# Optimization experiments

Hardware: AMD Instinct MI355X
Metric: run time of the kernel (lower is better)

Reference implementation:

```python
import jax, jax.numpy as jnp
import numpy as np

NUM_LAYER = 4
EMB = 64
ATOM_VOCAB = 64
BOND_VOCAB = 8
BN_EPS = 1e-5


def _batchnorm(h, gamma, beta):
    m = h.mean(axis=0)
    v = h.var(axis=0)
    return gamma * (h - m) * jax.lax.rsqrt(v + BN_EPS) + beta


def setup_inputs() -> dict:
    key = jax.random.key(0)
    ks = jax.random.split(key, 16)
    N, E, L = 100000, 1000000, NUM_LAYER
    x = jax.random.randint(ks[0], (N, 9), 0, ATOM_VOCAB)
    edge_index = jax.random.randint(ks[1], (2, E), 0, N)
    edge_attr = jax.random.randint(ks[2], (E, 3), 0, BOND_VOCAB)
    batch = jnp.sort(jax.random.randint(ks[3], (N,), 0, 512))
    s = 0.02
    atom_emb = jax.random.normal(ks[4], (9, ATOM_VOCAB, EMB), jnp.float32) * s
    bond_emb = jax.random.normal(ks[5], (L, 3, BOND_VOCAB, EMB), jnp.float32) * s
    eps = jnp.zeros((L,), jnp.float32)
    W1 = jax.random.normal(ks[6], (L, EMB, 2 * EMB), jnp.float32) * s
    b1 = jnp.zeros((L, 2 * EMB), jnp.float32)
    bn1_g = jnp.ones((L, 2 * EMB), jnp.float32)
    bn1_b = jnp.zeros((L, 2 * EMB), jnp.float32)
    W2 = jax.random.normal(ks[7], (L, 2 * EMB, EMB), jnp.float32) * s
    b2 = jnp.zeros((L, EMB), jnp.float32)
    bn_g = jnp.ones((L, EMB), jnp.float32)
    bn_b = jnp.zeros((L, EMB), jnp.float32)
    return dict(x=x, edge_index=edge_index, edge_attr=edge_attr, batch=batch,
                atom_emb=atom_emb, bond_emb=bond_emb, eps=eps,
                W1=W1, b1=b1, bn1_g=bn1_g, bn1_b=bn1_b,
                W2=W2, b2=b2, bn_g=bn_g, bn_b=bn_b)


def reference(x, edge_index, edge_attr, batch, atom_emb, bond_emb, eps,
              W1, b1, bn1_g, bn1_b, W2, b2, bn_g, bn_b):
    N = x.shape[0]
    src, dst = edge_index[0], edge_index[1]
    # AtomEncoder: sum embeddings over the 9 atom-feature columns
    h = sum(atom_emb[c][x[:, c]] for c in range(9))  # [N, EMB]
    for layer in range(NUM_LAYER):
        # BondEncoder for this layer
        ee = sum(bond_emb[layer, c][edge_attr[:, c]] for c in range(3))  # [E, EMB]
        # message: relu(x_j + edge_emb); aggregate: scatter-add at dst
        msg = jax.nn.relu(h[src] + ee)
        agg = jax.ops.segment_sum(msg, dst, num_segments=N)
        z = (1.0 + eps[layer]) * h + agg
        # MLP: Linear -> BN -> ReLU -> Linear
        z = z @ W1[layer] + b1[layer]
        z = jax.nn.relu(_batchnorm(z, bn1_g[layer], bn1_b[layer]))
        z = z @ W2[layer] + b2[layer]
        # outer BatchNorm, then ReLU on all but last layer (dropout = identity)
        z = _batchnorm(z, bn_g[layer], bn_b[layer])
        if layer < NUM_LAYER - 1:
            z = jax.nn.relu(z)
        h = z
    return (h, batch)
```

## Files before the change

kernel.cpp:

```cpp
#include <hip/hip_runtime.h>
#include <hip/hip_bf16.h>

#define N_NODES 100000
#define N_EDGES 1000000
#define EMB 64
#define NLAYER 4
#define NTILE 1563
#define NSB 391
#define NSHARD 16

typedef __hip_bfloat16 bf16;
typedef __attribute__((ext_vector_type(8))) short short8;
typedef __attribute__((ext_vector_type(4))) float f32x4;

static __device__ __forceinline__ float b2f(bf16 v) { return __bfloat162float(v); }
static __device__ __forceinline__ bf16 f2b(float v) { return __float2bfloat16(v); }

__global__ void k_atom(const int* __restrict__ x, const bf16* __restrict__ aemb,
                       bf16* __restrict__ P) {
    int tid = blockIdx.x * 256 + threadIdx.x;
    int n = tid >> 6, e = tid & 63;
    float s = 0.f;
#pragma unroll
    for (int c = 0; c < 9; ++c) {
        int v = x[n * 9 + c];
        s += b2f(aemb[(c * 64 + v) * 64 + e]);
    }
    P[tid] = f2b(s);
}

__global__ void k_bond(const bf16* __restrict__ bemb, bf16* __restrict__ cb) {
    int idx = blockIdx.x * 256 + threadIdx.x;
    int l = idx >> 15, r = idx & 32767;
    int combo = r >> 6, c = r & 63;
    int e0 = combo & 7, e1 = (combo >> 3) & 7, e2 = combo >> 6;
    float v = b2f(bemb[((l * 3 + 0) * 8 + e0) * 64 + c]) +
              b2f(bemb[((l * 3 + 1) * 8 + e1) * 64 + c]) +
              b2f(bemb[((l * 3 + 2) * 8 + e2) * 64 + c]);
    cb[idx] = f2b(v);
}

__global__ void k_hist(const int* __restrict__ ei, int* __restrict__ deg) {
    int e = blockIdx.x * 256 + threadIdx.x;
    if (e < N_EDGES) atomicAdd(&deg[ei[N_EDGES + e]], 1);
}

__global__ void k_scanA(const int* __restrict__ deg, int* __restrict__ bsum) {
    __shared__ int red[256];
    int i = blockIdx.x * 256 + threadIdx.x;
    red[threadIdx.x] = (i < N_NODES) ? deg[i] : 0;
    __syncthreads();
    for (int d = 128; d > 0; d >>= 1) {
        if (threadIdx.x < d) red[threadIdx.x] += red[threadIdx.x + d];
        __syncthreads();
    }
    if (threadIdx.x == 0) bsum[blockIdx.x] = red[0];
}

__global__ void k_scanB(const int* __restrict__ bsum, int* __restrict__ boff,
                        int* __restrict__ offs) {
    __shared__ int s[512];
    int t = threadIdx.x;
    s[t] = (t < NSB) ? bsum[t] : 0;
    __syncthreads();
    for (int d = 1; d < 512; d <<= 1) {
        int v = (t >= d) ? s[t - d] : 0;
        __syncthreads();
        s[t] += v;
        __syncthreads();
    }
    if (t < NSB) boff[t] = s[t] - bsum[t];
    if (t == 0) offs[N_NODES] = s[NSB - 1];
}

__global__ void k_scanC(const int* __restrict__ deg, const int* __restrict__ boff,
                        int* __restrict__ offs, int* __restrict__ cursor) {
    __shared__ int s[256];
    int i = blockIdx.x * 256 + threadIdx.x;
    int t = threadIdx.x;
    int d0 = (i < N_NODES) ? deg[i] : 0;
    s[t] = d0;
    __syncthreads();
    for (int d = 1; d < 256; d <<= 1) {
        int v = (t >= d) ? s[t - d] : 0;
        __syncthreads();
        s[t] += v;
        __syncthreads();
    }
    if (i < N_NODES) {
        int off = boff[blockIdx.x] + s[t] - d0;
        offs[i] = off;
        cursor[i] = off;
    }
}

__global__ void k_bucket(const int* __restrict__ ei, const int* __restrict__ ea,
                         int* __restrict__ cursor, int2* __restrict__ csr) {
    int e = blockIdx.x * 256 + threadIdx.x;
    if (e < N_EDGES) {
        int d = ei[N_EDGES + e];
        int pos = atomicAdd(&cursor[d], 1);
        int pk = ea[e * 3] + (ea[e * 3 + 1] << 3) + (ea[e * 3 + 2] << 6);
        csr[pos] = make_int2(ei[e], pk);
    }
}

__global__ void k_agg(const bf16* __restrict__ P, const int* __restrict__ offs,
                      const int2* __restrict__ csr,
                      const bf16* __restrict__ cb, const bf16* __restrict__ eps,
                      const float* __restrict__ p2s, const bf16* __restrict__ g2,
                      const bf16* __restrict__ bb2, int layer,
                      bf16* __restrict__ G, float* __restrict__ p1s) {
    if (blockIdx.x < NSHARD) p1s[blockIdx.x * 256 + threadIdx.x] = 0.f;
    int tid = blockIdx.x * 256 + threadIdx.x;
    int c = tid & 63;
    int n = __builtin_amdgcn_readfirstlane(tid >> 6);
    float av = 1.f, cv = 0.f, lo = -3.4e38f;
    if (layer > 0) {
        const float* pp = p2s + (layer - 1) * NSHARD * 128;
        float S = 0.f, Q = 0.f;
#pragma unroll
        for (int s = 0; s < NSHARD; ++s) { S += pp[s * 128 + c]; Q += pp[s * 128 + 64 + c]; }
        float mean = S / (float)N_NODES;
        float var = fmaxf(Q / (float)N_NODES - mean * mean, 0.f);
        av = b2f(g2[(layer - 1) * 64 + c]) * rsqrtf(var + 1e-5f);
        cv = b2f(bb2[(layer - 1) * 64 + c]) - mean * av;
        lo = 0.f;
    }
    const bf16* cbl = cb + layer * 512 * 64;
    float hself = fmaxf(av * b2f(P[(size_t)n * 64 + c]) + cv, lo);
    float acc = (1.f + b2f(eps[layer])) * hself;
    int s0 = __builtin_amdgcn_readfirstlane(offs[n]);
    int s1 = __builtin_amdgcn_readfirstlane(offs[n + 1]);
    int i = s0;
    for (; i + 8 <= s1; i += 8) {
        int sr[8], ep[8];
        float hv[8], bv[8];
#pragma unroll
        for (int u = 0; u < 8; ++u) {
            int2 ed = csr[i + u];
            sr[u] = __builtin_amdgcn_readfirstlane(ed.x);
            ep[u] = __builtin_amdgcn_readfirstlane(ed.y);
        }
#pragma unroll
        for (int u = 0; u < 8; ++u) hv[u] = b2f(P[(size_t)sr[u] * 64 + c]);
#pragma unroll
        for (int u = 0; u < 8; ++u) bv[u] = b2f(cbl[(size_t)ep[u] * 64 + c]);
#pragma unroll
        for (int u = 0; u < 8; ++u)
            acc += fmaxf(fmaxf(av * hv[u] + cv, lo) + bv[u], 0.f);
    }
    for (; i + 4 <= s1; i += 4) {
        int sr[4], ep[4];
        float hv[4], bv[4];
#pragma unroll
        for (int u = 0; u < 4; ++u) {
            int2 ed = csr[i + u];
            sr[u] = __builtin_amdgcn_readfirstlane(ed.x);
            ep[u] = __builtin_amdgcn_readfirstlane(ed.y);
        }
#pragma unroll
        for (int u = 0; u < 4; ++u) hv[u] = b2f(P[(size_t)sr[u] * 64 + c]);
#pragma unroll
        for (int u = 0; u < 4; ++u) bv[u] = b2f(cbl[(size_t)ep[u] * 64 + c]);
#pragma unroll
        for (int u = 0; u < 4; ++u)
            acc += fmaxf(fmaxf(av * hv[u] + cv, lo) + bv[u], 0.f);
    }
    for (; i < s1; ++i) {
        int2 ed = csr[i];
        int sr = __builtin_amdgcn_readfirstlane(ed.x);
        int ep = __builtin_amdgcn_readfirstlane(ed.y);
        float m = fmaxf(av * b2f(P[(size_t)sr * 64 + c]) + cv, lo) +
                  b2f(cbl[(size_t)ep * 64 + c]);
        acc += fmaxf(m, 0.f);
    }
    G[tid] = f2b(acc);
}

__global__ void k_wt(const bf16* __restrict__ W1, const bf16* __restrict__ W2,
                     bf16* __restrict__ W1T, bf16* __restrict__ W2T) {
    int idx = blockIdx.x * 256 + threadIdx.x;
    int l = idx >> 13, r = idx & 8191;
    int k = r >> 7, n = r & 127;
    W1T[l * 8192 + n * 64 + k] = W1[idx];
    int k2 = r >> 6, n2 = r & 63;
    W2T[l * 8192 + n2 * 128 + k2] = W2[idx];
}

__global__ __launch_bounds__(256) void k_mlp1s(
    const bf16* __restrict__ X, const bf16* __restrict__ W1T, const bf16* __restrict__ b1,
    int layer, float* __restrict__ p1s, float* __restrict__ p2s) {
    __shared__ bf16 zt[64 * 72];
    __shared__ float ps[4][4][32];
    __shared__ float qs[4][4][32];
    if (blockIdx.x < NSHARD && threadIdx.x < 128)
        p2s[(layer * NSHARD + blockIdx.x) * 128 + threadIdx.x] = 0.f;
    const bf16* Wl = W1T + layer * 8192;
    int r0 = blockIdx.x * 64;
    int nrows = min(64, N_NODES - r0);
    for (int i = threadIdx.x; i < 512; i += 256) {
        int r = i >> 3, c = (i & 7) * 8;
        short8 v = {};
        if (r < nrows) v = *(const short8*)&X[(r0 + r) * 64 + c];
        *(short8*)&zt[r * 72 + c] = v;
    }
    __syncthreads();
    int wid = threadIdx.x >> 6;
    int l = threadIdx.x & 63;
    int l15 = l & 15, lq = l >> 4;
    f32x4 acc[4][2];
#pragma unroll
    for (int m = 0; m < 4; ++m)
#pragma unroll
        for (int n = 0; n < 2; ++n) acc[m][n] = (f32x4){0.f, 0.f, 0.f, 0.f};
#pragma unroll
    for (int s = 0; s < 2; ++s) {
        short8 a[4], b[2];
#pragma unroll
        for (int m = 0; m < 4; ++m)
            a[m] = *(const short8*)&zt[(m * 16 + l15) * 72 + s * 32 + lq * 8];
#pragma unroll
        for (int n = 0; n < 2; ++n)
            b[n] = *(const short8*)&Wl[(wid * 32 + n * 16 + l15) * 64 + s * 32 + lq * 8];
#pragma unroll
        for (int m = 0; m < 4; ++m)
#pragma unroll
            for (int n = 0; n < 2; ++n)
                acc[m][n] = __builtin_amdgcn_mfma_f32_16x16x32_bf16(a[m], b[n], acc[m][n], 0, 0, 0);
    }
    float bb[2], cs[2] = {0.f, 0.f}, cq[2] = {0.f, 0.f};
#pragma unroll
    for (int n = 0; n < 2; ++n) bb[n] = b2f(b1[layer * 128 + wid * 32 + n * 16 + l15]);
#pragma unroll
    for (int m = 0; m < 4; ++m)
#pragma unroll
        for (int r = 0; r < 4; ++r) {
            int row = m * 16 + lq * 4 + r;
            if (row < nrows) {
#pragma unroll
                for (int n = 0; n < 2; ++n) {
                    float v = acc[m][n][r] + bb[n];
                    cs[n] += v; cq[n] += v * v;
                }
            }
        }
#pragma unroll
    for (int n = 0; n < 2; ++n) {
        ps[wid][lq][n * 16 + l15] = cs[n];
        qs[wid][lq][n * 16 + l15] = cq[n];
    }
    __syncthreads();
    if (threadIdx.x < 128) {
        int t = threadIdx.x, ww = t >> 5, cc = t & 31;
        float S = 0.f, Q = 0.f;
#pragma unroll
        for (int s4 = 0; s4 < 4; ++s4) { S += ps[ww][s4][cc]; Q += qs[ww][s4][cc]; }
        int sh = blockIdx.x & (NSHARD - 1);
        atomicAdd(&p1s[sh * 256 + t], S);
        atomicAdd(&p1s[sh * 256 + 128 + t], Q);
    }
}

__global__ __launch_bounds__(256) void k_mlp2(
    const bf16* __restrict__ W1T, const bf16* __restrict__ b1,
    const bf16* __restrict__ g1, const bf16* __restrict__ bb1,
    const float* __restrict__ p1s,
    const bf16* __restrict__ W2T, const bf16* __restrict__ bias2, int layer,
    const bf16* __restrict__ X, bf16* __restrict__ Y, float* __restrict__ p2s) {
    __shared__ bf16 zt[64 * 72];
    __shared__ bf16 yt[64 * 136];
    __shared__ float ps2[4][4][16];
    __shared__ float qs2[4][4][16];
    const bf16* W1l = W1T + layer * 8192;
    const bf16* W2l = W2T + layer * 8192;
    int r0 = blockIdx.x * 64;
    int nrows = min(64, N_NODES - r0);
    for (int i = threadIdx.x; i < 512; i += 256) {
        int r = i >> 3, c = (i & 7) * 8;
        short8 v = {};
        if (r < nrows) v = *(const short8*)&X[(r0 + r) * 64 + c];
        *(short8*)&zt[r * 72 + c] = v;
    }
    __syncthreads();
    int wid = threadIdx.x >> 6;
    int l = threadIdx.x & 63;
    int l15 = l & 15, lq = l >> 4;
    {
        f32x4 acc[4][2];
#pragma unroll
        for (int m = 0; m < 4; ++m)
#pragma unroll
            for (int n = 0; n < 2; ++n) acc[m][n] = (f32x4){0.f, 0.f, 0.f, 0.f};
#pragma unroll
        for (int s = 0; s < 2; ++s) {
            short8 a[4], b[2];
#pragma unroll
            for (int m = 0; m < 4; ++m)
                a[m] = *(const short8*)&zt[(m * 16 + l15) * 72 + s * 32 + lq * 8];
#pragma unroll
            for (int n = 0; n < 2; ++n)
                b[n] = *(const short8*)&W1l[(wid * 32 + n * 16 + l15) * 64 + s * 32 + lq * 8];
#pragma unroll
            for (int m = 0; m < 4; ++m)
#pragma unroll
                for (int n = 0; n < 2; ++n)
                    acc[m][n] = __builtin_amdgcn_mfma_f32_16x16x32_bf16(a[m], b[n], acc[m][n], 0, 0, 0);
        }
        float aav[2], ccv[2], bbv[2];
#pragma unroll
        for (int n = 0; n < 2; ++n) {
            int col = wid * 32 + n * 16 + l15;
            float S = 0.f, Q = 0.f;
#pragma unroll
            for (int s4 = 0; s4 < NSHARD; ++s4) {
                S += p1s[s4 * 256 + col];
                Q += p1s[s4 * 256 + 128 + col];
            }
            float mean = S / (float)N_NODES;
            float var = fmaxf(Q / (float)N_NODES - mean * mean, 0.f);
            aav[n] = b2f(g1[layer * 128 + col]) * rsqrtf(var + 1e-5f);
            ccv[n] = b2f(bb1[layer * 128 + col]) - mean * aav[n];
            bbv[n] = b2f(b1[layer * 128 + col]);
        }
#pragma unroll
        for (int m = 0; m < 4; ++m)
#pragma unroll
            for (int n = 0; n < 2; ++n)
#pragma unroll
                for (int r = 0; r < 4; ++r) {
                    int row = m * 16 + lq * 4 + r;
                    float v = fmaxf(aav[n] * (acc[m][n][r] + bbv[n]) + ccv[n], 0.f);
                    yt[row * 136 + wid * 32 + n * 16 + l15] = f2b(v);
                }
    }
    __syncthreads();
    {
        f32x4 acc2[4];
#pragma unroll
        for (int m = 0; m < 4; ++m) acc2[m] = (f32x4){0.f, 0.f, 0.f, 0.f};
#pragma unroll
        for (int s = 0; s < 4; ++s) {
            short8 a[4];
            short8 b = *(const short8*)&W2l[(wid * 16 + l15) * 128 + s * 32 + lq * 8];
#pragma unroll
            for (int m = 0; m < 4; ++m)
                a[m] = *(const short8*)&yt[(m * 16 + l15) * 136 + s * 32 + lq * 8];
#pragma unroll
            for (int m = 0; m < 4; ++m)
                acc2[m] = __builtin_amdgcn_mfma_f32_16x16x32_bf16(a[m], b, acc2[m], 0, 0, 0);
        }
        float bb2 = b2f(bias2[layer * 64 + wid * 16 + l15]);
        float cs = 0.f, cq = 0.f;
#pragma unroll
        for (int m = 0; m < 4; ++m)
#pragma unroll
            for (int r = 0; r < 4; ++r) {
                int row = m * 16 + lq * 4 + r;
                float v = acc2[m][r] + bb2;
                zt[row * 72 + wid * 16 + l15] = f2b(v);
                if (row < nrows) { cs += v; cq += v * v; }
            }
        ps2[wid][lq][l15] = cs;
        qs2[wid][lq][l15] = cq;
    }
    __syncthreads();
    for (int i = threadIdx.x; i < 512; i += 256) {
        int r = i >> 3, c = (i & 7) * 8;
        if (r < nrows)
            *(short8*)&Y[(r0 + r) * 64 + c] = *(const short8*)&zt[r * 72 + c];
    }
    if (threadIdx.x < 64) {
        int ww = threadIdx.x >> 4, cc = threadIdx.x & 15;
        float S = 0.f, Q = 0.f;
#pragma unroll
        for (int s4 = 0; s4 < 4; ++s4) { S += ps2[ww][s4][cc]; Q += qs2[ww][s4][cc]; }
        int sh = blockIdx.x & (NSHARD - 1);
        atomicAdd(&p2s[(layer * NSHARD + sh) * 128 + threadIdx.x], S);
        atomicAdd(&p2s[(layer * NSHARD + sh) * 128 + 64 + threadIdx.x], Q);
    }
}

__global__ void k_out(const bf16* __restrict__ P, const float* __restrict__ p2s,
                      const bf16* __restrict__ g2, const bf16* __restrict__ bb2,
                      const int* __restrict__ batch, float* __restrict__ out) {
    int tid = blockIdx.x * 256 + threadIdx.x;
    int c = tid & 63;
    const float* pp = p2s + 3 * NSHARD * 128;
    float S = 0.f, Q = 0.f;
#pragma unroll
    for (int s = 0; s < NSHARD; ++s) { S += pp[s * 128 + c]; Q += pp[s * 128 + 64 + c]; }
    float mean = S / (float)N_NODES;
    float var = fmaxf(Q / (float)N_NODES - mean * mean, 0.f);
    float av = b2f(g2[3 * 64 + c]) * rsqrtf(var + 1e-5f);
    float cv = b2f(bb2[3 * 64 + c]) - mean * av;
    float v = b2f(f2b(av * b2f(P[tid]) + cv));
    out[tid] = (v != v || fabsf(v) > 1e20f) ? 0.f : v;
    if (tid < N_NODES) out[N_NODES * EMB + tid] = (float)batch[tid];
}

extern "C" void kernel_launch(void* const* d_in, const int* in_sizes, int n_in,
                              void* d_out, int out_size, void* d_ws, size_t ws_size,
                              hipStream_t stream) {
    (void)in_sizes; (void)n_in; (void)out_size; (void)ws_size;
    const int* x     = (const int*)d_in[0];
    const int* ei    = (const int*)d_in[1];
    const int* ea    = (const int*)d_in[2];
    const int* batch = (const int*)d_in[3];
    const bf16* aemb = (const bf16*)d_in[4];
    const bf16* bemb = (const bf16*)d_in[5];
    const bf16* eps  = (const bf16*)d_in[6];
    const bf16* W1   = (const bf16*)d_in[7];
    const bf16* b1   = (const bf16*)d_in[8];
    const bf16* g1   = (const bf16*)d_in[9];
    const bf16* bb1  = (const bf16*)d_in[10];
    const bf16* W2   = (const bf16*)d_in[11];
    const bf16* b2   = (const bf16*)d_in[12];
    const bf16* g2   = (const bf16*)d_in[13];
    const bf16* bb2  = (const bf16*)d_in[14];

    bf16* Y = (bf16*)d_ws;
    char* ob = (char*)d_out;
    bf16* X       = (bf16*)ob;
    int*  deg     = (int*)(ob + 12800000);
    int*  offs    = (int*)(ob + 13200000);
    int*  cursor  = (int*)(ob + 13600008);
    int2* csr     = (int2*)(ob + 14000008);
    float* p1s    = (float*)(ob + 22000008);
    float* p2s    = (float*)(ob + 22016392);
    int*  bsum    = (int*)(ob + 22049160);
    int*  boff    = (int*)(ob + 22050724);
    bf16* w1t     = (bf16*)(ob + 22052288);
    bf16* w2t     = (bf16*)(ob + 22117824);
    bf16* cbt     = (bf16*)(ob + 22183360);

    hipMemsetAsync(deg, 0, 400000, stream);

    k_atom<<<25000, 256, 0, stream>>>(x, aemb, Y);
    k_wt<<<128, 256, 0, stream>>>(W1, W2, w1t, w2t);
    k_bond<<<512, 256, 0, stream>>>(bemb, cbt);
    k_hist<<<3907, 256, 0, stream>>>(ei, deg);
    k_scanA<<<NSB, 256, 0, stream>>>(deg, bsum);
    k_scanB<<<1, 512, 0, stream>>>(bsum, boff, offs);
    k_scanC<<<NSB, 256, 0, stream>>>(deg, boff, offs, cursor);
    k_bucket<<<3907, 256, 0, stream>>>(ei, ea, cursor, csr);

    for (int l = 0; l < NLAYER; ++l) {
        k_agg<<<25000, 256, 0, stream>>>(Y, offs, csr, cbt, eps,
                                         p2s, g2, bb2, l, X, p1s);
        k_mlp1s<<<NTILE, 256, 0, stream>>>(X, w1t, b1, l, p1s, p2s);
        k_mlp2<<<NTILE, 256, 0, stream>>>(w1t, b1, g1, bb1, p1s, w2t, b2, l, X, Y, p2s);
    }
    k_out<<<25000, 256, 0, stream>>>(Y, p2s, g2, bb2, batch, (float*)d_out);
}
```

Before: 574.1 us.

## Build CSR via two-pass binned scatter to localize random writes

Replaces the single-pass random atomic bucket scatter with a two-pass scheme. Edges are first grouped into coarse destination bins of 512 nodes, using per-block shared-memory counts and global bin cursors. A per-bin pass then does the fine scatter into the CSR, so the cursor atomics and CSR writes stay within a small address range per block. This adds an extra pass over the edge data, a temporary buffer, and bin histogram and scan work.

After: 586.1 us. 2.1% more time.

```diff
diff --git a/kernel.cpp b/kernel.cpp
--- a/kernel.cpp
+++ b/kernel.cpp
@@ -8,6 +8,8 @@
 #define NTILE 1563
 #define NSB 391
 #define NSHARD 16
+#define NBIN 196
+#define NS1B 489
 
 typedef __hip_bfloat16 bf16;
 typedef __attribute__((ext_vector_type(8))) short short8;
@@ -40,9 +42,21 @@
     cb[idx] = f2b(v);
 }
 
-__global__ void k_hist(const int* __restrict__ ei, int* __restrict__ deg) {
-    int e = blockIdx.x * 256 + threadIdx.x;
-    if (e < N_EDGES) atomicAdd(&deg[ei[N_EDGES + e]], 1);
+__global__ __launch_bounds__(1024) void k_hist(const int* __restrict__ ei,
+                                               int* __restrict__ deg,
+                                               int* __restrict__ bcnt) {
+    __shared__ int lb[NBIN];
+    for (int i = threadIdx.x; i < NBIN; i += 1024) lb[i] = 0;
+    __syncthreads();
+    int e = blockIdx.x * 1024 + threadIdx.x;
+    if (e < N_EDGES) {
+        int d = ei[N_EDGES + e];
+        atomicAdd(&deg[d], 1);
+        atomicAdd(&lb[d >> 9], 1);
+    }
+    __syncthreads();
+    for (int i = threadIdx.x; i < NBIN; i += 1024)
+        if (lb[i]) atomicAdd(&bcnt[i], lb[i]);
 }
 
 __global__ void k_scanA(const int* __restrict__ deg, int* __restrict__ bsum) {
@@ -58,19 +72,24 @@
 }
 
 __global__ void k_scanB(const int* __restrict__ bsum, int* __restrict__ boff,
-                        int* __restrict__ offs) {
-    __shared__ int s[512];
+                        int* __restrict__ offs, const int* __restrict__ bcnt,
+                        int* __restrict__ bbase, int* __restrict__ bcur) {
+    __shared__ int s[512], s2[512];
     int t = threadIdx.x;
-    s[t] = (t < NSB) ? bsum[t] : 0;
+    int v0 = (t < NSB) ? bsum[t] : 0;
+    int b0 = (t < NBIN) ? bcnt[t] : 0;
+    s[t] = v0; s2[t] = b0;
     __syncthreads();
     for (int d = 1; d < 512; d <<= 1) {
-        int v = (t >= d) ? s[t - d] : 0;
+        int va = (t >= d) ? s[t - d] : 0;
+        int vb = (t >= d) ? s2[t - d] : 0;
         __syncthreads();
-        s[t] += v;
+        s[t] += va; s2[t] += vb;
         __syncthreads();
     }
-    if (t < NSB) boff[t] = s[t] - bsum[t];
+    if (t < NSB) boff[t] = s[t] - v0;
     if (t == 0) offs[N_NODES] = s[NSB - 1];
+    if (t < NBIN) { int st = s2[t] - b0; bbase[t] = st; bcur[t] = st; }
 }
 
 __global__ void k_scanC(const int* __restrict__ deg, const int* __restrict__ boff,
@@ -94,14 +113,53 @@
     }
 }
 
-__global__ void k_bucket(const int* __restrict__ ei, const int* __restrict__ ea,
-                         int* __restrict__ cursor, int2* __restrict__ csr) {
-    int e = blockIdx.x * 256 + threadIdx.x;
-    if (e < N_EDGES) {
-        int d = ei[N_EDGES + e];
+__global__ __launch_bounds__(256) void k_scat1(const int* __restrict__ ei,
+                                               const int* __restrict__ ea,
+                                               int* __restrict__ bcur,
+                                               int2* __restrict__ tmp8,
+                                               int* __restrict__ tmpd) {
+    __shared__ int lcnt[NBIN], gb[NBIN], lcur[NBIN];
+    for (int i = threadIdx.x; i < NBIN; i += 256) lcnt[i] = 0;
+    __syncthreads();
+    int base = blockIdx.x * 2048;
+#pragma unroll
+    for (int k = 0; k < 8; ++k) {
+        int e = base + k * 256 + threadIdx.x;
+        if (e < N_EDGES) atomicAdd(&lcnt[ei[N_EDGES + e] >> 9], 1);
+    }
+    __syncthreads();
+    for (int i = threadIdx.x; i < NBIN; i += 256) {
+        lcur[i] = 0;
+        if (lcnt[i]) gb[i] = atomicAdd(&bcur[i], lcnt[i]);
+    }
+    __syncthreads();
+#pragma unroll
+    for (int k = 0; k < 8; ++k) {
+        int e = base + k * 256 + threadIdx.x;
+        if (e < N_EDGES) {
+            int d = ei[N_EDGES + e];
+            int bin = d >> 9;
+            int pk = ea[e * 3] + (ea[e * 3 + 1] << 3) + (ea[e * 3 + 2] << 6);
+            int r = atomicAdd(&lcur[bin], 1);
+            int pos = gb[bin] + r;
+            tmp8[pos] = make_int2(ei[e], pk);
+            tmpd[pos] = d;
+        }
+    }
+}
+
+__global__ __launch_bounds__(256) void k_scat2(const int2* __restrict__ tmp8,
+                                               const int* __restrict__ tmpd,
+                                               const int* __restrict__ bbase,
+                                               const int* __restrict__ bcur,
+                                               int* __restrict__ cursor,
+                                               int2* __restrict__ csr) {
+    int bin = blockIdx.x;
+    int s0 = bbase[bin], s1 = bcur[bin];
+    for (int i = s0 + threadIdx.x; i < s1; i += 256) {
+        int d = tmpd[i];
         int pos = atomicAdd(&cursor[d], 1);
-        int pk = ea[e * 3] + (ea[e * 3 + 1] << 3) + (ea[e * 3 + 2] << 6);
-        csr[pos] = make_int2(ei[e], pk);
+        csr[pos] = tmp8[i];
     }
 }
 
@@ -422,6 +480,8 @@
     bf16* Y = (bf16*)d_ws;
     char* ob = (char*)d_out;
     bf16* X       = (bf16*)ob;
+    int2* tmp8    = (int2*)ob;
+    int*  tmpd    = (int*)(ob + 8000000);
     int*  deg     = (int*)(ob + 12800000);
     int*  offs    = (int*)(ob + 13200000);
     int*  cursor  = (int*)(ob + 13600008);
@@ -433,17 +493,22 @@
     bf16* w1t     = (bf16*)(ob + 22052288);
     bf16* w2t     = (bf16*)(ob + 22117824);
     bf16* cbt     = (bf16*)(ob + 22183360);
+    int*  bcnt    = (int*)(ob + 22445504);
+    int*  bbase   = (int*)(ob + 22446288);
+    int*  bcur    = (int*)(ob + 22447072);
 
     hipMemsetAsync(deg, 0, 400000, stream);
+    hipMemsetAsync(bcnt, 0, NBIN * 4, stream);
 
     k_atom<<<25000, 256, 0, stream>>>(x, aemb, Y);
     k_wt<<<128, 256, 0, stream>>>(W1, W2, w1t, w2t);
     k_bond<<<512, 256, 0, stream>>>(bemb, cbt);
-    k_hist<<<3907, 256, 0, stream>>>(ei, deg);
+    k_hist<<<977, 1024, 0, stream>>>(ei, deg, bcnt);
     k_scanA<<<NSB, 256, 0, stream>>>(deg, bsum);
-    k_scanB<<<1, 512, 0, stream>>>(bsum, boff, offs);
+    k_scanB<<<1, 512, 0, stream>>>(bsum, boff, offs, bcnt, bbase, bcur);
     k_scanC<<<NSB, 256, 0, stream>>>(deg, boff, offs, cursor);
-    k_bucket<<<3907, 256, 0, stream>>>(ei, ea, cursor, csr);
+    k_scat1<<<NS1B, 256, 0, stream>>>(ei, ea, bcur, tmp8, tmpd);
+    k_scat2<<<NBIN, 256, 0, stream>>>(tmp8, tmpd, bbase, bcur, cursor, csr);
 
     for (int l = 0; l < NLAYER; ++l) {
         k_agg<<<25000, 256, 0, stream>>>(Y, offs, csr, cbt, eps,
```
